# Kernel optimization log

Measured on AMD Instinct MI355X. Metric: run time of the kernel, lower is better.

The kernel has to match this reference:

```python
import jax, jax.numpy as jnp
import numpy as np

E = 8          # num_experts
K = 2          # num_experts_per_tok
D = 1024       # d_model
F = 4096       # d_ff


def setup_inputs() -> dict:
    key = jax.random.key(0)
    k1, k2, k3, k4, k5 = jax.random.split(key, 5)
    s = 0.02
    return {
        "x": jax.random.normal(k1, (2, 2048, D), dtype=jnp.float32),
        "gate_w": jax.random.normal(k2, (D, E), dtype=jnp.float32) * s,
        "w1": jax.random.normal(k3, (E, D, F), dtype=jnp.float32) * s,
        "w2": jax.random.normal(k4, (E, F, D), dtype=jnp.float32) * s,
        "w3": jax.random.normal(k5, (E, D, F), dtype=jnp.float32) * s,
    }


def reference(x, gate_w, w1, w2, w3):
    # x: [B, S, D] -> squash to tokens [T, D]
    xs = x.reshape(-1, x.shape[-1])                      # [T, D]
    gate_logits = xs @ gate_w                            # [T, E]
    topw, sel = jax.lax.top_k(gate_logits, K)            # [T, K] each
    # softmax over the K selected logits in float32, cast back (matches torch code)
    topw = jax.nn.softmax(topw.astype(jnp.float32), axis=-1).astype(x.dtype)
    # per-token combine weight for every expert: zero where not selected [T, E]
    comb = (jax.nn.one_hot(sel, E, dtype=x.dtype) * topw[..., None]).sum(axis=1)
    out = jnp.zeros_like(xs)
    # loop over fixed small expert count (structurally distinct weights);
    # masked-dense combine is mathematically identical to the gather/scatter
    # in the original (weight is exactly 0 for unselected tokens)
    for i in range(E):
        h = jax.nn.silu(xs @ w1[i]) * (xs @ w3[i])       # [T, F] SwiGLU
        out = out + comb[:, i:i + 1] * (h @ w2[i])       # [T, D]
    return out.reshape(x.shape)
```

## Files before the change

### kernel.cpp

```cpp
#include <hip/hip_runtime.h>


#define T_TOK 4096
#define DM    1024
#define FF    4096
#define NE    8

#define BM 128
#define BN 128
#define BK 32
#define BS 36

typedef unsigned short u16;
typedef short short8 __attribute__((ext_vector_type(8)));
typedef float floatx4 __attribute__((ext_vector_type(4)));

#define WS_COUNTS  0u
#define WS_CURS    32u
#define WS_OFFS    64u
#define WS_SEL     4096u
#define WS_SELW    (4096u + 32768u)
#define WS_STOK    (4096u + 65536u)
#define WS_SW      (4096u + 98304u)
#define WS_XBF     (1u << 20)
#define WS_HBUF    ((1u << 20) + (8u << 20))

__device__ __forceinline__ u16 f2bf(float f) {
  union { float f; unsigned int u; } v; v.f = f;
  unsigned int r = v.u + 0x7fffu + ((v.u >> 16) & 1u);
  return (u16)(r >> 16);
}

__device__ __forceinline__ short8 ld_b_frag(const u16* p) {
  union { unsigned long long q[2]; short8 v; } r;
  r.q[0] = *(const unsigned long long*)(p);
  r.q[1] = *(const unsigned long long*)(p + 4);
  return r.v;
}

__global__ __launch_bounds__(256) void gate_kernel(
    const float* __restrict__ x, const float* __restrict__ gw,
    u16* __restrict__ xbf, int* __restrict__ sel, float* __restrict__ selw,
    int* __restrict__ counts)
{
  const int t = blockIdx.x * 4 + (threadIdx.x >> 6);
  const int lane = threadIdx.x & 63;
  const float* xr = x + (size_t)t * DM;
  double acc[NE];
#pragma unroll
  for (int e = 0; e < NE; ++e) acc[e] = 0.0;
#pragma unroll 4
  for (int i = 0; i < 16; ++i) {
    const int d = i * 64 + lane;
    const float xv = xr[d];
    xbf[(size_t)t * DM + d] = f2bf(xv);
    const float4* g = (const float4*)(gw + (size_t)d * NE);
    float4 g0 = g[0], g1 = g[1];
    acc[0] += (double)xv * g0.x; acc[1] += (double)xv * g0.y;
    acc[2] += (double)xv * g0.z; acc[3] += (double)xv * g0.w;
    acc[4] += (double)xv * g1.x; acc[5] += (double)xv * g1.y;
    acc[6] += (double)xv * g1.z; acc[7] += (double)xv * g1.w;
  }
#pragma unroll
  for (int off = 32; off >= 1; off >>= 1) {
#pragma unroll
    for (int e = 0; e < NE; ++e) acc[e] += __shfl_xor(acc[e], off, 64);
  }
  if (lane == 0) {
    int i1 = 0; double v1 = acc[0];
#pragma unroll
    for (int e = 1; e < NE; ++e) if (acc[e] > v1) { v1 = acc[e]; i1 = e; }
    int i2 = -1; double v2 = -1e300;
#pragma unroll
    for (int e = 0; e < NE; ++e) if (e != i1 && acc[e] > v2) { v2 = acc[e]; i2 = e; }
    float p1 = 1.0f / (1.0f + expf((float)(v2 - v1)));
    sel[t * 2] = i1; sel[t * 2 + 1] = i2;
    selw[t * 2] = p1; selw[t * 2 + 1] = 1.0f - p1;
    atomicAdd(&counts[i1], 1);
    atomicAdd(&counts[i2], 1);
  }
}

__global__ void offsets_kernel(const int* __restrict__ counts, int* __restrict__ offsets) {
  if (threadIdx.x == 0) {
    int s = 0;
#pragma unroll
    for (int e = 0; e < NE; ++e) { offsets[e] = s; s += counts[e]; }
  }
}

__global__ void fill_kernel(const int* __restrict__ sel, const float* __restrict__ selw,
                            const int* __restrict__ offsets, int* __restrict__ cursors,
                            int* __restrict__ stok, float* __restrict__ sw)
{
  const int t = blockIdx.x * blockDim.x + threadIdx.x;
  if (t >= T_TOK) return;
#pragma unroll
  for (int k = 0; k < 2; ++k) {
    int e = sel[t * 2 + k];
    int pos = atomicAdd(&cursors[e], 1);
    int p = offsets[e] + pos;
    stok[p] = t;
    sw[p] = selw[t * 2 + k];
  }
}

__global__ __launch_bounds__(256, 2) void gemm1_kernel(
    const u16* __restrict__ xbf, const float* __restrict__ w1, const float* __restrict__ w3,
    const int* __restrict__ stok, const int* __restrict__ offsets,
    const int* __restrict__ counts, u16* __restrict__ Hbuf)
{
  const int e  = blockIdx.z;
  const int mt = blockIdx.y;
  const int ne = counts[e];
  if (mt * BM >= ne) return;
  const int nt = blockIdx.x;
  const int base = offsets[e];
  const float* __restrict__ W1 = w1 + (size_t)e * DM * FF;
  const float* __restrict__ W3 = w3 + (size_t)e * DM * FF;

  __shared__ u16 Al[BM][BK];
  __shared__ u16 B1l[BN][BS];
  __shared__ u16 B3l[BN][BS];

  const int tid  = threadIdx.x;
  const int lane = tid & 63;
  const int wv   = tid >> 6;
  const int wm   = (wv & 1) * 64;
  const int wn   = (wv >> 1) * 64;
  const int ln15 = lane & 15;
  const int q    = lane >> 4;

  const int arow = tid >> 1;
  const int aseg = (tid & 1) * 16;
  const int rg_a = mt * BM + arow;
  const u16* asrc = nullptr;
  if (rg_a < ne) {
    int tok = stok[base + rg_a];
    asrc = xbf + (size_t)tok * DM + aseg;
  }

  const int nb = tid & 127;
  const int kh = (tid >> 7) * 16;
  const int n0 = nt * BN;
  const float* b1p = W1 + (size_t)kh * FF + n0 + nb;
  const float* b3p = W3 + (size_t)kh * FF + n0 + nb;

  floatx4 acc1[4][4], acc3[4][4];
#pragma unroll
  for (int mi = 0; mi < 4; ++mi)
#pragma unroll
    for (int ni = 0; ni < 4; ++ni) {
      acc1[mi][ni] = (floatx4){0.f, 0.f, 0.f, 0.f};
      acc3[mi][ni] = (floatx4){0.f, 0.f, 0.f, 0.f};
    }

  for (int kc = 0; kc < DM; kc += BK) {
    if (asrc) {
      const uint4* s = (const uint4*)(asrc + kc);
      *(uint4*)&Al[arow][aseg]     = s[0];
      *(uint4*)&Al[arow][aseg + 8] = s[1];
    } else {
      uint4 z = {0u, 0u, 0u, 0u};
      *(uint4*)&Al[arow][aseg]     = z;
      *(uint4*)&Al[arow][aseg + 8] = z;
    }
    const float* p1 = b1p + (size_t)kc * FF;
    const float* p3 = b3p + (size_t)kc * FF;
#pragma unroll
    for (int kk = 0; kk < 16; kk += 4) {
      union { u16 s[4]; uint2 u; } v1, v3;
#pragma unroll
      for (int j = 0; j < 4; ++j) {
        v1.s[j] = f2bf(p1[(size_t)(kk + j) * FF]);
        v3.s[j] = f2bf(p3[(size_t)(kk + j) * FF]);
      }
      *(uint2*)&B1l[nb][kh + kk] = v1.u;
      *(uint2*)&B3l[nb][kh + kk] = v3.u;
    }
    __syncthreads();

    short8 af[4];
#pragma unroll
    for (int mi = 0; mi < 4; ++mi)
      af[mi] = *(const short8*)&Al[wm + mi * 16 + ln15][q * 8];
#pragma unroll
    for (int ni = 0; ni < 4; ++ni) {
      short8 b1 = ld_b_frag(&B1l[wn + ni * 16 + ln15][q * 8]);
      short8 b3 = ld_b_frag(&B3l[wn + ni * 16 + ln15][q * 8]);
#pragma unroll
      for (int mi = 0; mi < 4; ++mi) {
        acc1[mi][ni] = __builtin_amdgcn_mfma_f32_16x16x32_bf16(af[mi], b1, acc1[mi][ni], 0, 0, 0);
        acc3[mi][ni] = __builtin_amdgcn_mfma_f32_16x16x32_bf16(af[mi], b3, acc3[mi][ni], 0, 0, 0);
      }
    }
    __syncthreads();
  }

#pragma unroll
  for (int mi = 0; mi < 4; ++mi) {
#pragma unroll
    for (int reg = 0; reg < 4; ++reg) {
      int rg = mt * BM + wm + mi * 16 + q * 4 + reg;
      if (rg < ne) {
        u16* dst = Hbuf + (size_t)(base + rg) * FF + n0 + wn + ln15;
#pragma unroll
        for (int ni = 0; ni < 4; ++ni) {
          float a = acc1[mi][ni][reg];
          float b = acc3[mi][ni][reg];
          float h = (a / (1.0f + __expf(-a))) * b;
          dst[ni * 16] = f2bf(h);
        }
      }
    }
  }
}

__global__ __launch_bounds__(256, 2) void gemm2_kernel(
    const u16* __restrict__ Hbuf, const float* __restrict__ w2,
    const int* __restrict__ stok, const float* __restrict__ sw,
    const int* __restrict__ offsets, const int* __restrict__ counts,
    float* __restrict__ out)
{
  const int e  = blockIdx.z;
  const int mt = blockIdx.y;
  const int ne = counts[e];
  if (mt * BM >= ne) return;
  const int nt = blockIdx.x;
  const int base = offsets[e];
  const float* __restrict__ W2 = w2 + (size_t)e * FF * DM;

  __shared__ u16 Al[BM][BK];
  __shared__ u16 Bl[BN][BS];

  const int tid  = threadIdx.x;
  const int lane = tid & 63;
  const int wv   = tid >> 6;
  const int wm   = (wv & 1) * 64;
  const int wn   = (wv >> 1) * 64;
  const int ln15 = lane & 15;
  const int q    = lane >> 4;

  const int arow = tid >> 1;
  const int aseg = (tid & 1) * 16;
  const int rg_a = mt * BM + arow;
  const u16* asrc = nullptr;
  if (rg_a < ne) asrc = Hbuf + (size_t)(base + rg_a) * FF + aseg;

  const int nb = tid & 127;
  const int kh = (tid >> 7) * 16;
  const int n0 = nt * BN;
  const float* bp = W2 + (size_t)kh * DM + n0 + nb;

  floatx4 acc[4][4];
#pragma unroll
  for (int mi = 0; mi < 4; ++mi)
#pragma unroll
    for (int ni = 0; ni < 4; ++ni) acc[mi][ni] = (floatx4){0.f, 0.f, 0.f, 0.f};

  for (int kc = 0; kc < FF; kc += BK) {
    if (asrc) {
      const uint4* s = (const uint4*)(asrc + kc);
      *(uint4*)&Al[arow][aseg]     = s[0];
      *(uint4*)&Al[arow][aseg + 8] = s[1];
    } else {
      uint4 z = {0u, 0u, 0u, 0u};
      *(uint4*)&Al[arow][aseg]     = z;
      *(uint4*)&Al[arow][aseg + 8] = z;
    }
    const float* p2 = bp + (size_t)kc * DM;
#pragma unroll
    for (int kk = 0; kk < 16; kk += 4) {
      union { u16 s[4]; uint2 u; } v2;
#pragma unroll
      for (int j = 0; j < 4; ++j) v2.s[j] = f2bf(p2[(size_t)(kk + j) * DM]);
      *(uint2*)&Bl[nb][kh + kk] = v2.u;
    }
    __syncthreads();

    short8 af[4];
#pragma unroll
    for (int mi = 0; mi < 4; ++mi)
      af[mi] = *(const short8*)&Al[wm + mi * 16 + ln15][q * 8];
#pragma unroll
    for (int ni = 0; ni < 4; ++ni) {
      short8 b = ld_b_frag(&Bl[wn + ni * 16 + ln15][q * 8]);
#pragma unroll
      for (int mi = 0; mi < 4; ++mi)
        acc[mi][ni] = __builtin_amdgcn_mfma_f32_16x16x32_bf16(af[mi], b, acc[mi][ni], 0, 0, 0);
    }
    __syncthreads();
  }

#pragma unroll
  for (int mi = 0; mi < 4; ++mi) {
#pragma unroll
    for (int reg = 0; reg < 4; ++reg) {
      int rg = mt * BM + wm + mi * 16 + q * 4 + reg;
      if (rg < ne) {
        int p = base + rg;
        int tok = stok[p];
        float wgt = sw[p];
        float* dst = out + (size_t)tok * DM + n0 + wn + ln15;
#pragma unroll
        for (int ni = 0; ni < 4; ++ni)
          atomicAdd(&dst[ni * 16], wgt * acc[mi][ni][reg]);
      }
    }
  }
}

extern "C" void kernel_launch(void* const* d_in, const int* in_sizes, int n_in,
                              void* d_out, int out_size, void* d_ws, size_t ws_size,
                              hipStream_t stream) {
  const float* x  = (const float*)d_in[0];
  const float* gw = (const float*)d_in[1];
  const float* w1 = (const float*)d_in[2];
  const float* w2 = (const float*)d_in[3];
  const float* w3 = (const float*)d_in[4];
  float* out = (float*)d_out;
  char* ws = (char*)d_ws;

  int*   counts  = (int*)(ws + WS_COUNTS);
  int*   cursors = (int*)(ws + WS_CURS);
  int*   offsets = (int*)(ws + WS_OFFS);
  int*   sel     = (int*)(ws + WS_SEL);
  float* selw    = (float*)(ws + WS_SELW);
  int*   stok    = (int*)(ws + WS_STOK);
  float* sw      = (float*)(ws + WS_SW);
  u16*   xbf     = (u16*)(ws + WS_XBF);
  u16*   Hbuf    = (u16*)(ws + WS_HBUF);

  size_t need = (size_t)WS_HBUF + (size_t)(T_TOK * 2) * FF * 2;
  if (ws_size < need) return;

  hipMemsetAsync(ws, 0, 96, stream);
  hipMemsetAsync(d_out, 0, (size_t)T_TOK * DM * sizeof(float), stream);

  gate_kernel<<<T_TOK / 4, 256, 0, stream>>>(x, gw, xbf, sel, selw, counts);
  offsets_kernel<<<1, 64, 0, stream>>>(counts, offsets);
  fill_kernel<<<T_TOK / 256, 256, 0, stream>>>(sel, selw, offsets, cursors, stok, sw);
  gemm1_kernel<<<dim3(FF / BN, T_TOK / BM, NE), 256, 0, stream>>>(xbf, w1, w3, stok, offsets, counts, Hbuf);
  gemm2_kernel<<<dim3(DM / BN, T_TOK / BM, NE), 256, 0, stream>>>(Hbuf, w2, stok, sw, offsets, counts, out);
}
```

Before: 1.050 ms.

## Pre-transpose weights to bf16, use async LDS loads, split-K gemm2 with combine

Adds kernels that transpose and convert w1/w3 (interleaved into one matrix) and w2 to bf16 K-major layout each call. The expert GEMMs then load tiles directly into swizzled LDS with global_load_lds, with no per-element strided fp32 loads or in-loop conversions. gemm2 is split into two K halves that write bf16 partials, and a combine kernel sums them and applies the gate weights instead of using atomics. The cost is an extra pass over all weights every call, additional workspace, and bf16 rounding of the partial outputs.

```diff
diff --git a/kernel.cpp b/kernel.cpp
--- a/kernel.cpp
+++ b/kernel.cpp
@@ -9,7 +9,6 @@
 #define BM 128
 #define BN 128
 #define BK 32
-#define BS 36
 
 typedef unsigned short u16;
 typedef short short8 __attribute__((ext_vector_type(8)));
@@ -22,8 +21,12 @@
 #define WS_SELW    (4096u + 32768u)
 #define WS_STOK    (4096u + 65536u)
 #define WS_SW      (4096u + 98304u)
-#define WS_XBF     (1u << 20)
-#define WS_HBUF    ((1u << 20) + (8u << 20))
+#define WS_PMAP    (4096u + 131072u)
+#define WS_XBF     ((size_t)1 << 20)
+#define WS_HBUF    ((size_t)9 << 20)
+#define WS_W13     ((size_t)73 << 20)
+#define WS_WT2     ((size_t)201 << 20)
+#define WS_YBUF    ((size_t)73 << 20)
 
 __device__ __forceinline__ u16 f2bf(float f) {
   union { float f; unsigned int u; } v; v.f = f;
@@ -31,11 +34,15 @@
   return (u16)(r >> 16);
 }
 
-__device__ __forceinline__ short8 ld_b_frag(const u16* p) {
-  union { unsigned long long q[2]; short8 v; } r;
-  r.q[0] = *(const unsigned long long*)(p);
-  r.q[1] = *(const unsigned long long*)(p + 4);
-  return r.v;
+__device__ __forceinline__ float bf2f(u16 h) {
+  union { unsigned int u; float f; } v; v.u = ((unsigned int)h) << 16;
+  return v.f;
+}
+
+__device__ __forceinline__ void async16(u16* lds, const u16* g) {
+  __builtin_amdgcn_global_load_lds(
+      (const __attribute__((address_space(1))) unsigned int*)g,
+      (__attribute__((address_space(3))) unsigned int*)lds, 16, 0, 0);
 }
 
 __global__ __launch_bounds__(256) void gate_kernel(
@@ -89,9 +96,9 @@
   }
 }
 
-__global__ void fill_kernel(const int* __restrict__ sel, const float* __restrict__ selw,
+__global__ void fill_kernel(const int* __restrict__ sel,
                             const int* __restrict__ offsets, int* __restrict__ cursors,
-                            int* __restrict__ stok, float* __restrict__ sw)
+                            int* __restrict__ stok, int* __restrict__ pmap)
 {
   const int t = blockIdx.x * blockDim.x + threadIdx.x;
   if (t >= T_TOK) return;
@@ -101,12 +108,70 @@
     int pos = atomicAdd(&cursors[e], 1);
     int p = offsets[e] + pos;
     stok[p] = t;
-    sw[p] = selw[t * 2 + k];
-  }
-}
-
-__global__ __launch_bounds__(256, 2) void gemm1_kernel(
-    const u16* __restrict__ xbf, const float* __restrict__ w1, const float* __restrict__ w3,
+    pmap[t * 2 + k] = p;
+  }
+}
+
+__global__ __launch_bounds__(256) void convt13_kernel(const float* __restrict__ w1,
+                                                      const float* __restrict__ w3,
+                                                      u16* __restrict__ dst)
+{
+  __shared__ float tile[64][65];
+  const int e = blockIdx.z >> 1;
+  const int s = blockIdx.z & 1;
+  const float* src = (s ? w3 : w1) + (size_t)e * DM * FF;
+  u16* d = dst + (size_t)e * (2 * FF) * DM;
+  const int f0 = blockIdx.x * 64;
+  const int k0 = blockIdx.y * 64;
+  const int tr = threadIdx.x >> 4;
+  const int tc = (threadIdx.x & 15) * 4;
+#pragma unroll
+  for (int i = 0; i < 64; i += 16) {
+    const float4 v = *(const float4*)&src[(size_t)(k0 + tr + i) * FF + f0 + tc];
+    tile[tr + i][tc]     = v.x; tile[tr + i][tc + 1] = v.y;
+    tile[tr + i][tc + 2] = v.z; tile[tr + i][tc + 3] = v.w;
+  }
+  __syncthreads();
+  const int nbase = f0 * 2 + s * 16;
+#pragma unroll
+  for (int ii = 0; ii < 64; ii += 16) {
+    union { u16 q[4]; uint2 u; } o;
+#pragma unroll
+    for (int j = 0; j < 4; ++j) o.q[j] = f2bf(tile[tc + j][tr + ii]);
+    const int nrow = nbase + ii * 2 + tr;
+    *(uint2*)&d[(size_t)nrow * DM + k0 + tc] = o.u;
+  }
+}
+
+__global__ __launch_bounds__(256) void convt2_kernel(const float* __restrict__ src,
+                                                     u16* __restrict__ dst)
+{
+  __shared__ float tile[64][65];
+  const int e = blockIdx.z;
+  src += (size_t)e * FF * DM;
+  dst += (size_t)e * FF * DM;
+  const int n0 = blockIdx.x * 64;
+  const int k0 = blockIdx.y * 64;
+  const int tr = threadIdx.x >> 4;
+  const int tc = (threadIdx.x & 15) * 4;
+#pragma unroll
+  for (int i = 0; i < 64; i += 16) {
+    const float4 v = *(const float4*)&src[(size_t)(k0 + tr + i) * DM + n0 + tc];
+    tile[tr + i][tc]     = v.x; tile[tr + i][tc + 1] = v.y;
+    tile[tr + i][tc + 2] = v.z; tile[tr + i][tc + 3] = v.w;
+  }
+  __syncthreads();
+#pragma unroll
+  for (int i = 0; i < 64; i += 16) {
+    union { u16 q[4]; uint2 u; } o;
+#pragma unroll
+    for (int j = 0; j < 4; ++j) o.q[j] = f2bf(tile[tc + j][tr + i]);
+    *(uint2*)&dst[(size_t)(n0 + tr + i) * FF + k0 + tc] = o.u;
+  }
+}
+
+__global__ __launch_bounds__(256, 2) void gemm1p_kernel(
+    const u16* __restrict__ xbf, const u16* __restrict__ w13,
     const int* __restrict__ stok, const int* __restrict__ offsets,
     const int* __restrict__ counts, u16* __restrict__ Hbuf)
 {
@@ -116,12 +181,10 @@
   if (mt * BM >= ne) return;
   const int nt = blockIdx.x;
   const int base = offsets[e];
-  const float* __restrict__ W1 = w1 + (size_t)e * DM * FF;
-  const float* __restrict__ W3 = w3 + (size_t)e * DM * FF;
-
-  __shared__ u16 Al[BM][BK];
-  __shared__ u16 B1l[BN][BS];
-  __shared__ u16 B3l[BN][BS];
+  const u16* __restrict__ W = w13 + (size_t)e * (2 * FF) * DM;
+
+  __shared__ u16 Al[BM * BK];
+  __shared__ u16 Bl[BN * BK];
 
   const int tid  = threadIdx.x;
   const int lane = tid & 63;
@@ -130,108 +193,88 @@
   const int wn   = (wv >> 1) * 64;
   const int ln15 = lane & 15;
   const int q    = lane >> 4;
-
-  const int arow = tid >> 1;
-  const int aseg = (tid & 1) * 16;
-  const int rg_a = mt * BM + arow;
-  const u16* asrc = nullptr;
-  if (rg_a < ne) {
-    int tok = stok[base + rg_a];
-    asrc = xbf + (size_t)tok * DM + aseg;
-  }
-
-  const int nb = tid & 127;
-  const int kh = (tid >> 7) * 16;
-  const int n0 = nt * BN;
-  const float* b1p = W1 + (size_t)kh * FF + n0 + nb;
-  const float* b3p = W3 + (size_t)kh * FF + n0 + nb;
-
-  floatx4 acc1[4][4], acc3[4][4];
+  const int n0   = nt * BN;
+
+  const int rsub  = lane >> 2;
+  const int slog  = (lane & 3) ^ ((rsub >> 1) & 3);
+  const int seg   = slog * 8;
+
+  const u16* ag[2]; const u16* bg[2];
+#pragma unroll
+  for (int it = 0; it < 2; ++it) {
+    int r  = wv * 32 + it * 16 + rsub;
+    int rg = mt * BM + r;
+    int p  = base + (rg < ne ? rg : 0);
+    int tok = stok[p];
+    ag[it] = xbf + (size_t)tok * DM + seg;
+    bg[it] = W + (size_t)(n0 + r) * DM + seg;
+  }
+  u16* al[2] = { Al + (wv * 32) * BK, Al + (wv * 32 + 16) * BK };
+  u16* bl[2] = { Bl + (wv * 32) * BK, Bl + (wv * 32 + 16) * BK };
+
+  const int swz = (ln15 >> 1) & 3;
+
+  floatx4 acc[4][4];
 #pragma unroll
   for (int mi = 0; mi < 4; ++mi)
 #pragma unroll
+    for (int ni = 0; ni < 4; ++ni) acc[mi][ni] = (floatx4){0.f, 0.f, 0.f, 0.f};
+
+  for (int kc = 0; kc < DM; kc += BK) {
+    async16(al[0], ag[0] + kc); async16(al[1], ag[1] + kc);
+    async16(bl[0], bg[0] + kc); async16(bl[1], bg[1] + kc);
+    __syncthreads();
+
+    short8 af[4];
+#pragma unroll
+    for (int mi = 0; mi < 4; ++mi)
+      af[mi] = *(const short8*)&Al[(wm + mi * 16 + ln15) * BK + ((q ^ swz) * 8)];
+#pragma unroll
     for (int ni = 0; ni < 4; ++ni) {
-      acc1[mi][ni] = (floatx4){0.f, 0.f, 0.f, 0.f};
-      acc3[mi][ni] = (floatx4){0.f, 0.f, 0.f, 0.f};
-    }
-
-  for (int kc = 0; kc < DM; kc += BK) {
-    if (asrc) {
-      const uint4* s = (const uint4*)(asrc + kc);
-      *(uint4*)&Al[arow][aseg]     = s[0];
-      *(uint4*)&Al[arow][aseg + 8] = s[1];
-    } else {
-      uint4 z = {0u, 0u, 0u, 0u};
-      *(uint4*)&Al[arow][aseg]     = z;
-      *(uint4*)&Al[arow][aseg + 8] = z;
-    }
-    const float* p1 = b1p + (size_t)kc * FF;
-    const float* p3 = b3p + (size_t)kc * FF;
-#pragma unroll
-    for (int kk = 0; kk < 16; kk += 4) {
-      union { u16 s[4]; uint2 u; } v1, v3;
-#pragma unroll
-      for (int j = 0; j < 4; ++j) {
-        v1.s[j] = f2bf(p1[(size_t)(kk + j) * FF]);
-        v3.s[j] = f2bf(p3[(size_t)(kk + j) * FF]);
-      }
-      *(uint2*)&B1l[nb][kh + kk] = v1.u;
-      *(uint2*)&B3l[nb][kh + kk] = v3.u;
+      short8 bf = *(const short8*)&Bl[(wn + ni * 16 + ln15) * BK + ((q ^ swz) * 8)];
+#pragma unroll
+      for (int mi = 0; mi < 4; ++mi)
+        acc[mi][ni] = __builtin_amdgcn_mfma_f32_16x16x32_bf16(af[mi], bf, acc[mi][ni], 0, 0, 0);
     }
     __syncthreads();
-
-    short8 af[4];
-#pragma unroll
-    for (int mi = 0; mi < 4; ++mi)
-      af[mi] = *(const short8*)&Al[wm + mi * 16 + ln15][q * 8];
-#pragma unroll
-    for (int ni = 0; ni < 4; ++ni) {
-      short8 b1 = ld_b_frag(&B1l[wn + ni * 16 + ln15][q * 8]);
-      short8 b3 = ld_b_frag(&B3l[wn + ni * 16 + ln15][q * 8]);
-#pragma unroll
-      for (int mi = 0; mi < 4; ++mi) {
-        acc1[mi][ni] = __builtin_amdgcn_mfma_f32_16x16x32_bf16(af[mi], b1, acc1[mi][ni], 0, 0, 0);
-        acc3[mi][ni] = __builtin_amdgcn_mfma_f32_16x16x32_bf16(af[mi], b3, acc3[mi][ni], 0, 0, 0);
-      }
-    }
-    __syncthreads();
-  }
-
+  }
+
+  const int hbase = (n0 + wn) >> 1;
 #pragma unroll
   for (int mi = 0; mi < 4; ++mi) {
 #pragma unroll
     for (int reg = 0; reg < 4; ++reg) {
       int rg = mt * BM + wm + mi * 16 + q * 4 + reg;
       if (rg < ne) {
-        u16* dst = Hbuf + (size_t)(base + rg) * FF + n0 + wn + ln15;
-#pragma unroll
-        for (int ni = 0; ni < 4; ++ni) {
-          float a = acc1[mi][ni][reg];
-          float b = acc3[mi][ni][reg];
+        u16* dst = Hbuf + (size_t)(base + rg) * FF + hbase + ln15;
+#pragma unroll
+        for (int j = 0; j < 2; ++j) {
+          float a = acc[mi][2 * j][reg];
+          float b = acc[mi][2 * j + 1][reg];
           float h = (a / (1.0f + __expf(-a))) * b;
-          dst[ni * 16] = f2bf(h);
+          dst[j * 16] = f2bf(h);
         }
       }
     }
   }
 }
 
-__global__ __launch_bounds__(256, 2) void gemm2_kernel(
-    const u16* __restrict__ Hbuf, const float* __restrict__ w2,
-    const int* __restrict__ stok, const float* __restrict__ sw,
+__global__ __launch_bounds__(256, 2) void gemm2p_kernel(
+    const u16* __restrict__ Hbuf, const u16* __restrict__ wt2,
     const int* __restrict__ offsets, const int* __restrict__ counts,
-    float* __restrict__ out)
-{
-  const int e  = blockIdx.z;
+    u16* __restrict__ Ybuf)
+{
+  const int e    = blockIdx.z >> 1;
+  const int half = blockIdx.z & 1;
   const int mt = blockIdx.y;
   const int ne = counts[e];
   if (mt * BM >= ne) return;
   const int nt = blockIdx.x;
   const int base = offsets[e];
-  const float* __restrict__ W2 = w2 + (size_t)e * FF * DM;
-
-  __shared__ u16 Al[BM][BK];
-  __shared__ u16 Bl[BN][BS];
+  const u16* __restrict__ W2 = wt2 + (size_t)e * FF * DM;
+
+  __shared__ u16 Al[BM * BK];
+  __shared__ u16 Bl[BN * BK];
 
   const int tid  = threadIdx.x;
   const int lane = tid & 63;
@@ -240,17 +283,25 @@
   const int wn   = (wv >> 1) * 64;
   const int ln15 = lane & 15;
   const int q    = lane >> 4;
-
-  const int arow = tid >> 1;
-  const int aseg = (tid & 1) * 16;
-  const int rg_a = mt * BM + arow;
-  const u16* asrc = nullptr;
-  if (rg_a < ne) asrc = Hbuf + (size_t)(base + rg_a) * FF + aseg;
-
-  const int nb = tid & 127;
-  const int kh = (tid >> 7) * 16;
-  const int n0 = nt * BN;
-  const float* bp = W2 + (size_t)kh * DM + n0 + nb;
+  const int n0   = nt * BN;
+
+  const int rsub = lane >> 2;
+  const int slog = (lane & 3) ^ ((rsub >> 1) & 3);
+  const int seg  = slog * 8;
+
+  const u16* ag[2]; const u16* bg[2];
+#pragma unroll
+  for (int it = 0; it < 2; ++it) {
+    int r  = wv * 32 + it * 16 + rsub;
+    int rg = mt * BM + r;
+    int p  = base + (rg < ne ? rg : 0);
+    ag[it] = Hbuf + (size_t)p * FF + seg;
+    bg[it] = W2 + (size_t)(n0 + r) * FF + seg;
+  }
+  u16* al[2] = { Al + (wv * 32) * BK, Al + (wv * 32 + 16) * BK };
+  u16* bl[2] = { Bl + (wv * 32) * BK, Bl + (wv * 32 + 16) * BK };
+
+  const int swz = (ln15 >> 1) & 3;
 
   floatx4 acc[4][4];
 #pragma unroll
@@ -258,56 +309,66 @@
 #pragma unroll
     for (int ni = 0; ni < 4; ++ni) acc[mi][ni] = (floatx4){0.f, 0.f, 0.f, 0.f};
 
-  for (int kc = 0; kc < FF; kc += BK) {
-    if (asrc) {
-      const uint4* s = (const uint4*)(asrc + kc);
-      *(uint4*)&Al[arow][aseg]     = s[0];
-      *(uint4*)&Al[arow][aseg + 8] = s[1];
-    } else {
-      uint4 z = {0u, 0u, 0u, 0u};
-      *(uint4*)&Al[arow][aseg]     = z;
-      *(uint4*)&Al[arow][aseg + 8] = z;
-    }
-    const float* p2 = bp + (size_t)kc * DM;
-#pragma unroll
-    for (int kk = 0; kk < 16; kk += 4) {
-      union { u16 s[4]; uint2 u; } v2;
-#pragma unroll
-      for (int j = 0; j < 4; ++j) v2.s[j] = f2bf(p2[(size_t)(kk + j) * DM]);
-      *(uint2*)&Bl[nb][kh + kk] = v2.u;
+  const int kbeg = half * (FF / 2);
+  const int kend = kbeg + FF / 2;
+  for (int kc = kbeg; kc < kend; kc += BK) {
+    async16(al[0], ag[0] + kc); async16(al[1], ag[1] + kc);
+    async16(bl[0], bg[0] + kc); async16(bl[1], bg[1] + kc);
+    __syncthreads();
+
+    short8 af[4];
+#pragma unroll
+    for (int mi = 0; mi < 4; ++mi)
+      af[mi] = *(const short8*)&Al[(wm + mi * 16 + ln15) * BK + ((q ^ swz) * 8)];
+#pragma unroll
+    for (int ni = 0; ni < 4; ++ni) {
+      short8 bf = *(const short8*)&Bl[(wn + ni * 16 + ln15) * BK + ((q ^ swz) * 8)];
+#pragma unroll
+      for (int mi = 0; mi < 4; ++mi)
+        acc[mi][ni] = __builtin_amdgcn_mfma_f32_16x16x32_bf16(af[mi], bf, acc[mi][ni], 0, 0, 0);
     }
     __syncthreads();
-
-    short8 af[4];
-#pragma unroll
-    for (int mi = 0; mi < 4; ++mi)
-      af[mi] = *(const short8*)&Al[wm + mi * 16 + ln15][q * 8];
-#pragma unroll
-    for (int ni = 0; ni < 4; ++ni) {
-      short8 b = ld_b_frag(&Bl[wn + ni * 16 + ln15][q * 8]);
-#pragma unroll
-      for (int mi = 0; mi < 4; ++mi)
-        acc[mi][ni] = __builtin_amdgcn_mfma_f32_16x16x32_bf16(af[mi], b, acc[mi][ni], 0, 0, 0);
-    }
-    __syncthreads();
-  }
-
+  }
+
+  u16* Yb = Ybuf + (size_t)half * (2 * T_TOK) * DM;
 #pragma unroll
   for (int mi = 0; mi < 4; ++mi) {
 #pragma unroll
     for (int reg = 0; reg < 4; ++reg) {
       int rg = mt * BM + wm + mi * 16 + q * 4 + reg;
       if (rg < ne) {
-        int p = base + rg;
-        int tok = stok[p];
-        float wgt = sw[p];
-        float* dst = out + (size_t)tok * DM + n0 + wn + ln15;
+        u16* dst = Yb + (size_t)(base + rg) * DM + n0 + wn + ln15;
 #pragma unroll
         for (int ni = 0; ni < 4; ++ni)
-          atomicAdd(&dst[ni * 16], wgt * acc[mi][ni][reg]);
+          dst[ni * 16] = f2bf(acc[mi][ni][reg]);
       }
     }
   }
+}
+
+__global__ __launch_bounds__(256) void combine_kernel(
+    const u16* __restrict__ Ybuf, const int* __restrict__ pmap,
+    const float* __restrict__ selw, float* __restrict__ out)
+{
+  const int t = blockIdx.x;
+  const int c = threadIdx.x * 4;
+  const int p0 = pmap[t * 2], p1 = pmap[t * 2 + 1];
+  const float w0 = selw[t * 2], w1 = selw[t * 2 + 1];
+  const size_t HALF = (size_t)(2 * T_TOK) * DM;
+  const u16* a0 = Ybuf + (size_t)p0 * DM + c;
+  const u16* a1 = Ybuf + (size_t)p1 * DM + c;
+  union { u16 q[4]; uint2 u; } va0, vb0, va1, vb1;
+  va0.u = *(const uint2*)a0;
+  vb0.u = *(const uint2*)(a0 + HALF);
+  va1.u = *(const uint2*)a1;
+  vb1.u = *(const uint2*)(a1 + HALF);
+  float4 o;
+  float* op = &o.x;
+#pragma unroll
+  for (int j = 0; j < 4; ++j)
+    op[j] = w0 * (bf2f(va0.q[j]) + bf2f(vb0.q[j])) +
+            w1 * (bf2f(va1.q[j]) + bf2f(vb1.q[j]));
+  *(float4*)&out[(size_t)t * DM + c] = o;
 }
 
 extern "C" void kernel_launch(void* const* d_in, const int* in_sizes, int n_in,
@@ -327,19 +388,28 @@
   int*   sel     = (int*)(ws + WS_SEL);
   float* selw    = (float*)(ws + WS_SELW);
   int*   stok    = (int*)(ws + WS_STOK);
-  float* sw      = (float*)(ws + WS_SW);
+  int*   pmap    = (int*)(ws + WS_PMAP);
   u16*   xbf     = (u16*)(ws + WS_XBF);
   u16*   Hbuf    = (u16*)(ws + WS_HBUF);
-
-  size_t need = (size_t)WS_HBUF + (size_t)(T_TOK * 2) * FF * 2;
+  u16*   W13     = (u16*)(ws + WS_W13);
+  u16*   Wt2     = (u16*)(ws + WS_WT2);
+  u16*   Ybuf    = (u16*)(ws + WS_YBUF);
+
+  const size_t need = (size_t)265 << 20;
   if (ws_size < need) return;
 
   hipMemsetAsync(ws, 0, 96, stream);
-  hipMemsetAsync(d_out, 0, (size_t)T_TOK * DM * sizeof(float), stream);
 
   gate_kernel<<<T_TOK / 4, 256, 0, stream>>>(x, gw, xbf, sel, selw, counts);
   offsets_kernel<<<1, 64, 0, stream>>>(counts, offsets);
-  fill_kernel<<<T_TOK / 256, 256, 0, stream>>>(sel, selw, offsets, cursors, stok, sw);
-  gemm1_kernel<<<dim3(FF / BN, T_TOK / BM, NE), 256, 0, stream>>>(xbf, w1, w3, stok, offsets, counts, Hbuf);
-  gemm2_kernel<<<dim3(DM / BN, T_TOK / BM, NE), 256, 0, stream>>>(Hbuf, w2, stok, sw, offsets, counts, out);
-}
+  fill_kernel<<<T_TOK / 256, 256, 0, stream>>>(sel, offsets, cursors, stok, pmap);
+
+  convt13_kernel<<<dim3(FF / 64, DM / 64, NE * 2), 256, 0, stream>>>(w1, w3, W13);
+  convt2_kernel<<<dim3(DM / 64, FF / 64, NE), 256, 0, stream>>>(w2, Wt2);
+
+  gemm1p_kernel<<<dim3(2 * FF / BN, T_TOK / BM, NE), 256, 0, stream>>>(
+      xbf, W13, stok, offsets, counts, Hbuf);
+  gemm2p_kernel<<<dim3(DM / BN, T_TOK / BM, NE * 2), 256, 0, stream>>>(
+      Hbuf, Wt2, offsets, counts, Ybuf);
+  combine_kernel<<<T_TOK, 256, 0, stream>>>(Ybuf, pmap, selw, out);
+}
```

Measured after the change: 849.2 us. -19.1%, faster.
